# Optimization experiments

Measured on AMD Instinct MI355X. Metric: run time of the kernel, lower is better.

Reference implementation:

```python
import jax, jax.numpy as jnp
import numpy as np


def setup_inputs() -> dict:
    key = jax.random.key(0)
    B, C, D, H, W = 8, 2, 128, 96, 128
    corr = jax.random.normal(key, (B, C, D, H, W), dtype=jnp.float32)
    return {"corr": corr, "maxdisp": 50, "is_ux": 1}


def reference(corr, maxdisp, is_ux):
    # corr: (B, C, D, H, W). For each pixel (i, j) and displacement dx in
    # [-maxdisp, maxdisp], linearly interpolate corr along the D axis at
    # position (j + dx) if is_ux else (i + dx), with zero padding outside
    # [0, D-1] (matches grid_sample bilinear, align_corners=True, H==1).
    B, C, D, H, W = corr.shape
    K = 2 * maxdisp + 1
    dx = jnp.linspace(-float(maxdisp), float(maxdisp), K)  # (K,)
    if is_ux:
        base = jnp.broadcast_to(jnp.arange(W, dtype=jnp.float32)[None, :], (H, W))
    else:
        base = jnp.broadcast_to(jnp.arange(H, dtype=jnp.float32)[:, None], (H, W))
    pos = base[None, :, :] + dx[:, None, None]           # (K, H, W)
    i0f = jnp.floor(pos)
    w1 = (pos - i0f).astype(corr.dtype)                  # lerp weight for upper tap
    i0 = i0f.astype(jnp.int32)
    i1 = i0 + 1
    m0 = ((i0 >= 0) & (i0 < D)).astype(corr.dtype)       # zero-padding masks
    m1 = ((i1 >= 0) & (i1 < D)).astype(corr.dtype)
    idx0 = jnp.clip(i0, 0, D - 1)[None, None]            # (1,1,K,H,W) -> broadcast
    idx1 = jnp.clip(i1, 0, D - 1)[None, None]
    g0 = jnp.take_along_axis(corr, idx0, axis=2)         # (B, C, K, H, W)
    g1 = jnp.take_along_axis(corr, idx1, axis=2)
    out = g0 * ((1.0 - w1) * m0)[None, None] + g1 * (w1 * m1)[None, None]
    return out  # (B, C, 2*maxdisp+1, H, W)
```

## Files before the change

### kernel.cpp

```cpp
#include <hip/hip_runtime.h>


#define B_ 8
#define C_ 2
#define D_ 128
#define H_ 96
#define W_ 128
#define WT 32
#define NT 256

__global__ __launch_bounds__(NT, 8) void corr2cost_kernel(
    const float* __restrict__ corr,
    const int* __restrict__ maxdisp_p,
    const int* __restrict__ isux_p,
    float* __restrict__ out) {
  __shared__ float lds[D_ * WT];

  const int t   = threadIdx.x;
  const int bid = blockIdx.x;
  const int wt   = bid & (W_ / WT - 1);
  const int rest = bid >> 2;
  const int h    = rest % H_;
  const int bc   = rest / H_;
  const int w0   = wt * WT;
  const int HW   = H_ * W_;

  const int m     = *maxdisp_p;
  const int is_ux = *isux_p;
  const int K     = 2 * m + 1;

  int dlo = (is_ux ? w0 : h) - m;
  int dhi = (is_ux ? w0 + WT - 1 : h) + m + 1;
  dlo = dlo > 0 ? dlo : 0;
  dhi = dhi < D_ - 1 ? dhi : D_ - 1;

  const float* __restrict__ src =
      corr + (size_t)bc * D_ * HW + (size_t)h * W_ + w0;
  const int r0 = t >> 3;
  const int c4 = (t & 7) * 4;
  for (int r = dlo + r0; r <= dhi; r += 32) {
    *reinterpret_cast<float4*>(&lds[(r - dlo) * WT + c4]) =
        *reinterpret_cast<const float4*>(src + (size_t)r * HW + c4);
  }
  __syncthreads();

  const int wi   = t & (WT - 1);
  const int kg   = t >> 5;
  const int base = is_ux ? (w0 + wi) : h;

  float* __restrict__ dst =
      out + (size_t)bc * K * HW + (size_t)h * W_ + w0 + wi;

  for (int k = kg; k < K; k += NT / WT) {
    const float posf = (float)(base + k - m);
    const float i0f  = floorf(posf);
    const float w1   = posf - i0f;
    const int   i0   = (int)i0f;
    const int   i1   = i0 + 1;
    const float g0 = (i0 >= 0 && i0 < D_) ? lds[(i0 - dlo) * WT + wi] : 0.0f;
    const float g1 = (i1 >= 0 && i1 < D_) ? lds[(i1 - dlo) * WT + wi] : 0.0f;
    dst[(size_t)k * HW] = g0 * (1.0f - w1) + g1 * w1;
  }
}

extern "C" void kernel_launch(void* const* d_in, const int* in_sizes, int n_in,
                              void* d_out, int out_size, void* d_ws, size_t ws_size,
                              hipStream_t stream) {
  const float* corr    = (const float*)d_in[0];
  const int*   maxdisp = (const int*)d_in[1];
  const int*   is_ux   = (const int*)d_in[2];
  float*       out     = (float*)d_out;

  const int grid = B_ * C_ * H_ * (W_ / WT);
  corr2cost_kernel<<<grid, NT, 0, stream>>>(corr, maxdisp, is_ux, out);
}
```

Measured before the change: 174.7 us.

## Make blocks persistent over six tiles with double-buffered register-prefetched LDS loads

Each block now handles six row tiles of 64 columns with 512 threads. While it computes the current tile, it prefetches the next tile's 128 D-rows into registers, then writes them into the alternate LDS buffer. This aims to overlap global loads with output writes and to amortise block launch cost. In exchange it loads the full D range instead of only the window the displacements need (more read traffic), uses double the LDS, and launches fewer blocks, which lowers parallelism. The index clamping is also made branchless.

```diff
diff --git a/kernel.cpp b/kernel.cpp
--- a/kernel.cpp
+++ b/kernel.cpp
@@ -6,60 +6,101 @@
 #define D_ 128
 #define H_ 96
 #define W_ 128
-#define WT 32
-#define NT 256
+#define WT 64
+#define NHALF (W_ / WT)
+#define NTILES (B_ * C_ * H_ * NHALF)
+#define NT 512
+#define TPB 6
+#define NBLK (NTILES / TPB)
 
-__global__ __launch_bounds__(NT, 8) void corr2cost_kernel(
+__global__ __launch_bounds__(NT, 4) void corr2cost_kernel(
     const float* __restrict__ corr,
     const int* __restrict__ maxdisp_p,
     const int* __restrict__ isux_p,
     float* __restrict__ out) {
-  __shared__ float lds[D_ * WT];
+  __shared__ float lds[2][D_ * WT];
 
-  const int t   = threadIdx.x;
-  const int bid = blockIdx.x;
-  const int wt   = bid & (W_ / WT - 1);
-  const int rest = bid >> 2;
-  const int h    = rest % H_;
-  const int bc   = rest / H_;
-  const int w0   = wt * WT;
-  const int HW   = H_ * W_;
-
+  const int t     = threadIdx.x;
   const int m     = *maxdisp_p;
   const int is_ux = *isux_p;
   const int K     = 2 * m + 1;
+  const int HW    = H_ * W_;
 
-  int dlo = (is_ux ? w0 : h) - m;
-  int dhi = (is_ux ? w0 + WT - 1 : h) + m + 1;
-  dlo = dlo > 0 ? dlo : 0;
-  dhi = dhi < D_ - 1 ? dhi : D_ - 1;
+  const int r0 = t >> 4;
+  const int c4 = (t & 15) * 4;
+  const int T0 = blockIdx.x * TPB;
 
-  const float* __restrict__ src =
-      corr + (size_t)bc * D_ * HW + (size_t)h * W_ + w0;
-  const int r0 = t >> 3;
-  const int c4 = (t & 7) * 4;
-  for (int r = dlo + r0; r <= dhi; r += 32) {
-    *reinterpret_cast<float4*>(&lds[(r - dlo) * WT + c4]) =
-        *reinterpret_cast<const float4*>(src + (size_t)r * HW + c4);
+  float4 pf[4];
+
+  {
+    const int T    = T0;
+    const int half = T & (NHALF - 1);
+    const int sl   = T / NHALF;
+    const int h    = sl % H_;
+    const int bc   = sl / H_;
+    const float* src =
+        corr + (size_t)bc * D_ * HW + (size_t)h * W_ + half * WT + c4;
+#pragma unroll
+    for (int j = 0; j < 4; ++j)
+      pf[j] = *reinterpret_cast<const float4*>(src + (size_t)(j * 32 + r0) * HW);
+#pragma unroll
+    for (int j = 0; j < 4; ++j)
+      *reinterpret_cast<float4*>(&lds[0][(j * 32 + r0) * WT + c4]) = pf[j];
   }
   __syncthreads();
 
-  const int wi   = t & (WT - 1);
-  const int kg   = t >> 5;
-  const int base = is_ux ? (w0 + wi) : h;
+  for (int i = 0; i < TPB; ++i) {
+    const int cur = i & 1;
 
-  float* __restrict__ dst =
-      out + (size_t)bc * K * HW + (size_t)h * W_ + w0 + wi;
+    if (i + 1 < TPB) {
+      const int T    = T0 + i + 1;
+      const int half = T & (NHALF - 1);
+      const int sl   = T / NHALF;
+      const int h    = sl % H_;
+      const int bc   = sl / H_;
+      const float* src =
+          corr + (size_t)bc * D_ * HW + (size_t)h * W_ + half * WT + c4;
+#pragma unroll
+      for (int j = 0; j < 4; ++j)
+        pf[j] = *reinterpret_cast<const float4*>(src + (size_t)(j * 32 + r0) * HW);
+    }
 
-  for (int k = kg; k < K; k += NT / WT) {
-    const float posf = (float)(base + k - m);
-    const float i0f  = floorf(posf);
-    const float w1   = posf - i0f;
-    const int   i0   = (int)i0f;
-    const int   i1   = i0 + 1;
-    const float g0 = (i0 >= 0 && i0 < D_) ? lds[(i0 - dlo) * WT + wi] : 0.0f;
-    const float g1 = (i1 >= 0 && i1 < D_) ? lds[(i1 - dlo) * WT + wi] : 0.0f;
-    dst[(size_t)k * HW] = g0 * (1.0f - w1) + g1 * w1;
+    {
+      const int T    = T0 + i;
+      const int half = T & (NHALF - 1);
+      const int sl   = T / NHALF;
+      const int h    = sl % H_;
+      const int bc   = sl / H_;
+      const int wi   = t & (WT - 1);
+      const int kg   = t >> 6;
+      const int w    = half * WT + wi;
+      const int base = is_ux ? w : h;
+      const float* L = lds[cur];
+      float* dst = out + (size_t)bc * K * HW + (size_t)h * W_ + w;
+
+      for (int k = kg; k < K; k += NT / WT) {
+        const float posf = (float)(base + k - m);
+        const float i0f  = floorf(posf);
+        const float w1   = posf - i0f;
+        const int   i0   = (int)i0f;
+        const int   i1   = i0 + 1;
+        const float m0 = (i0 >= 0 && i0 < D_) ? 1.0f : 0.0f;
+        const float m1 = (i1 >= 0 && i1 < D_) ? 1.0f : 0.0f;
+        const int i0c = i0 < 0 ? 0 : (i0 > D_ - 1 ? D_ - 1 : i0);
+        const int i1c = i1 < 0 ? 0 : (i1 > D_ - 1 ? D_ - 1 : i1);
+        const float g0 = L[i0c * WT + wi];
+        const float g1 = L[i1c * WT + wi];
+        dst[(size_t)k * HW] = g0 * ((1.0f - w1) * m0) + g1 * (w1 * m1);
+      }
+    }
+
+    if (i + 1 < TPB) {
+      float* Ln = lds[cur ^ 1];
+#pragma unroll
+      for (int j = 0; j < 4; ++j)
+        *reinterpret_cast<float4*>(&Ln[(j * 32 + r0) * WT + c4]) = pf[j];
+    }
+    __syncthreads();
   }
 }
 
@@ -71,6 +112,5 @@
   const int*   is_ux   = (const int*)d_in[2];
   float*       out     = (float*)d_out;
 
-  const int grid = B_ * C_ * H_ * (W_ / WT);
-  corr2cost_kernel<<<grid, NT, 0, stream>>>(corr, maxdisp, is_ux, out);
+  corr2cost_kernel<<<NBLK, NT, 0, stream>>>(corr, maxdisp, is_ux, out);
 }
```

New measurement: 181.1 us. 3.7% more time.

## Retile over width halves and displacement chunks, drop lerp for integer shifts

Applied to the files above, without the earlier changes.

Each block now covers a 64-wide row segment and one 32-displacement chunk of K, with a grid remap that spreads consecutive blocks across XCDs. Only the D rows that chunk needs are staged into padded LDS. The interpolation is replaced by a direct gather, since integer positions always give a zero weight for the upper tap. This cuts redundant global loads and ALU work and raises the block count. It hard-codes at most 128 displacements (NKT*KC) and relies on integer maxdisp, and a large maxdisp could overflow the fixed MAXR LDS rows.

```diff
diff --git a/kernel.cpp b/kernel.cpp
--- a/kernel.cpp
+++ b/kernel.cpp
@@ -6,60 +6,74 @@
 #define D_ 128
 #define H_ 96
 #define W_ 128
-#define WT 32
-#define NT 256
+#define WT 64
+#define KC 32
+#define NKT 4
+#define NT 512
+#define RS 68
+#define MAXR 96
 
 __global__ __launch_bounds__(NT, 8) void corr2cost_kernel(
     const float* __restrict__ corr,
-    const int* __restrict__ maxdisp_p,
-    const int* __restrict__ isux_p,
+    const int* __restrict__ mp,
+    const int* __restrict__ up,
     float* __restrict__ out) {
-  __shared__ float lds[D_ * WT];
+  __shared__ float lds[MAXR * RS];
 
-  const int t   = threadIdx.x;
-  const int bid = blockIdx.x;
-  const int wt   = bid & (W_ / WT - 1);
-  const int rest = bid >> 2;
-  const int h    = rest % H_;
-  const int bc   = rest / H_;
-  const int w0   = wt * WT;
-  const int HW   = H_ * W_;
+  const int cpx = gridDim.x >> 3;
+  const int raw = blockIdx.x;
+  const int bid = (raw & 7) * cpx + (raw >> 3);
 
-  const int m     = *maxdisp_p;
-  const int is_ux = *isux_p;
-  const int K     = 2 * m + 1;
+  const int kt    = bid & (NKT - 1);
+  const int whalf = (bid >> 2) & 1;
+  const int sl    = bid >> 3;
+  const int h     = sl % H_;
+  const int bc    = sl / H_;
 
-  int dlo = (is_ux ? w0 : h) - m;
-  int dhi = (is_ux ? w0 + WT - 1 : h) + m + 1;
-  dlo = dlo > 0 ? dlo : 0;
-  dhi = dhi < D_ - 1 ? dhi : D_ - 1;
+  const int t  = threadIdx.x;
+  const int m  = *mp;
+  const int ux = *up;
+  const int K  = 2 * m + 1;
+  const int HW = H_ * W_;
+  const int w0 = whalf * WT;
+  const int k0 = kt * KC;
+
+  const int bmin = ux ? w0 : h;
+  const int bmax = ux ? (w0 + WT - 1) : h;
+  const int khi  = (k0 + KC - 1 < K - 1) ? (k0 + KC - 1) : (K - 1);
+  const int dlo  = bmin + k0 - m;
+  const int dhi  = bmax + khi - m;
+  const int dlo_c = dlo > 0 ? dlo : 0;
+  const int dhi_c = dhi < D_ - 1 ? dhi : D_ - 1;
+  const int R = dhi_c - dlo_c + 1;
 
   const float* __restrict__ src =
       corr + (size_t)bc * D_ * HW + (size_t)h * W_ + w0;
-  const int r0 = t >> 3;
-  const int c4 = (t & 7) * 4;
-  for (int r = dlo + r0; r <= dhi; r += 32) {
-    *reinterpret_cast<float4*>(&lds[(r - dlo) * WT + c4]) =
-        *reinterpret_cast<const float4*>(src + (size_t)r * HW + c4);
+  const int nf4 = R * (WT / 4);
+  for (int i = t; i < nf4; i += NT) {
+    const int r  = i >> 4;
+    const int w4 = (i & 15) * 4;
+    const float4 v =
+        *reinterpret_cast<const float4*>(src + (size_t)(dlo_c + r) * HW + w4);
+    *reinterpret_cast<float4*>(&lds[r * RS + w4]) = v;
   }
   __syncthreads();
 
   const int wi   = t & (WT - 1);
-  const int kg   = t >> 5;
-  const int base = is_ux ? (w0 + wi) : h;
-
+  const int kg   = t >> 6;
+  const int base = ux ? (w0 + wi) : h;
   float* __restrict__ dst =
       out + (size_t)bc * K * HW + (size_t)h * W_ + w0 + wi;
 
-  for (int k = kg; k < K; k += NT / WT) {
-    const float posf = (float)(base + k - m);
-    const float i0f  = floorf(posf);
-    const float w1   = posf - i0f;
-    const int   i0   = (int)i0f;
-    const int   i1   = i0 + 1;
-    const float g0 = (i0 >= 0 && i0 < D_) ? lds[(i0 - dlo) * WT + wi] : 0.0f;
-    const float g1 = (i1 >= 0 && i1 < D_) ? lds[(i1 - dlo) * WT + wi] : 0.0f;
-    dst[(size_t)k * HW] = g0 * (1.0f - w1) + g1 * w1;
+#pragma unroll
+  for (int j = 0; j < KC / 8; ++j) {
+    const int k = k0 + kg + j * 8;
+    const int d = base + k - m;
+    const bool ok = (unsigned)d < (unsigned)D_;
+    int ld = d - dlo_c;
+    ld = ld < 0 ? 0 : (ld > MAXR - 1 ? MAXR - 1 : ld);
+    const float val = ok ? lds[ld * RS + wi] : 0.0f;
+    if (k < K) dst[(size_t)k * HW] = val;
   }
 }
 
@@ -71,6 +85,6 @@
   const int*   is_ux   = (const int*)d_in[2];
   float*       out     = (float*)d_out;
 
-  const int grid = B_ * C_ * H_ * (W_ / WT);
+  const int grid = B_ * C_ * H_ * 2 * NKT;
   corr2cost_kernel<<<grid, NT, 0, stream>>>(corr, maxdisp, is_ux, out);
 }
```

New measurement: 180.2 us. 1.03x slower.
